# Kernel optimization log

Measured on AMD Instinct MI355X. Metric: run time of the kernel, lower is better.

The kernel has to match this reference:

```python
import jax, jax.numpy as jnp
import numpy as np

B, C, D = 16, 128, 256


def setup_inputs() -> dict:
    key = jax.random.key(0)
    ks = jax.random.split(key, 12)
    s = 0.05
    return {
        "h_t": jax.random.normal(ks[0], (B, C, D), jnp.float32),
        "A_a": jax.random.normal(ks[1], (C, C), jnp.float32) * s,
        "A_m": jax.random.normal(ks[2], (C, C), jnp.float32) * s,
        "W1": jax.random.normal(ks[3], (2 * D, D), jnp.float32) * s,
        "b1": jax.random.normal(ks[4], (D,), jnp.float32) * s,
        "W2": jax.random.normal(ks[5], (D, 1), jnp.float32) * s,
        "b2": jax.random.normal(ks[6], (1,), jnp.float32) * s,
        "Wa": jax.random.normal(ks[7], (D, D), jnp.float32) * s,
        "ba": jax.random.normal(ks[8], (D,), jnp.float32) * s,
        "Wm": jax.random.normal(ks[9], (D, D), jnp.float32) * s,
        "bm": jax.random.normal(ks[10], (D,), jnp.float32) * s,
        "beta1": jnp.float32(1.0),
        "beta2": jnp.float32(1.0),
        "beta3": jnp.float32(1.0),
    }


def reference(h_t, A_a, A_m, W1, b1, W2, b2, Wa, ba, Wm, bm, beta1, beta2, beta3):
    d = h_t.shape[-1]
    # Pairwise edge-MLP score S[b,u,v] = sigmoid(W2 @ relu(W1 @ [h_u; h_v] + b1) + b2).
    # Split W1 into the half acting on h_u and the half acting on h_v, so the
    # (B,C,C,2D) concat never materializes (same math as Linear on the concat).
    pre_u = jnp.einsum('bud,dk->buk', h_t, W1[:d])        # (B,C,D)
    pre_v = jnp.einsum('bvd,dk->bvk', h_t, W1[d:])        # (B,C,D)
    hidden = jax.nn.relu(pre_u[:, :, None, :] + pre_v[:, None, :, :] + b1)  # (B,C,C,D)
    S = jax.nn.sigmoid(jnp.einsum('buvk,ko->buvo', hidden, W2)[..., 0] + b2[0])  # (B,C,C)

    # Additive aggregation: a_t[b,v,:] = sum_u (S*A_a)[b,u,v] * h_t[b,u,:]
    a_t = jnp.einsum('buv,bud->bvd', S * A_a, h_t)

    # Hadamard aggregation: m_t[b,v,d] = sum_u A_m[u,v] * h[b,u,d] * h[b,v,d]
    #                              = (A_m^T @ h_t) * h_t  (avoids (B,C,C,D) tensor)
    m_t = jnp.einsum('uv,bud->bvd', A_m, h_t) * h_t

    z_t = (beta1 * h_t
           + beta2 * (jnp.einsum('bvd,de->bve', a_t, Wa) + ba)
           + beta3 * (jnp.einsum('bvd,de->bve', m_t, Wm) + bm))
    return z_t
```

## Files before the change

### kernel.cpp

```cpp
#include <hip/hip_runtime.h>

#define B_ 16
#define C_ 128
#define D_ 256

__global__ __launch_bounds__(256) void k1_pq(const float* __restrict__ h,
                                             const float* __restrict__ W1,
                                             const float* __restrict__ b1,
                                             float* __restrict__ P,
                                             float* __restrict__ Q) {
  const int tid = threadIdx.x;
  const int col = blockIdx.x * 64 + (tid & 63);
  const int rbase = (tid >> 6) * 8;
  const int row0 = blockIdx.y * 32;
  __shared__ float hs[32][D_];
#pragma unroll
  for (int r = 0; r < 32; ++r) hs[r][tid] = h[(row0 + r) * D_ + tid];
  __syncthreads();

  const int c = col & 255;
  const float* Wcol = W1 + c + ((col & 256) << 8);

  float acc[8];
#pragma unroll
  for (int i = 0; i < 8; ++i) acc[i] = 0.f;

#pragma unroll 2
  for (int d = 0; d < D_; d += 4) {
    const float w0 = Wcol[(d + 0) * D_];
    const float w1 = Wcol[(d + 1) * D_];
    const float w2 = Wcol[(d + 2) * D_];
    const float w3 = Wcol[(d + 3) * D_];
#pragma unroll
    for (int i = 0; i < 8; ++i) {
      const float4 hv = *(const float4*)&hs[rbase + i][d];
      acc[i] = fmaf(hv.x, w0, acc[i]);
      acc[i] = fmaf(hv.y, w1, acc[i]);
      acc[i] = fmaf(hv.z, w2, acc[i]);
      acc[i] = fmaf(hv.w, w3, acc[i]);
    }
  }

  if (col < 256) {
#pragma unroll
    for (int i = 0; i < 8; ++i) P[(row0 + rbase + i) * D_ + c] = acc[i];
  } else {
    const float bb = b1[c];
#pragma unroll
    for (int i = 0; i < 8; ++i) Q[(row0 + rbase + i) * D_ + c] = acc[i] + bb;
  }
}

__global__ __launch_bounds__(256) void k2_s(const float* __restrict__ P,
                                            const float* __restrict__ Q,
                                            const float* __restrict__ W2,
                                            const float* __restrict__ b2,
                                            const float* __restrict__ Aa,
                                            float* __restrict__ SA) {
  const int b = blockIdx.z;
  const int u0 = blockIdx.x * 32;
  const int v0 = blockIdx.y * 32;
  const int tid = threadIdx.x;
  const int tx = tid & 15;
  const int ty = tid >> 4;
  __shared__ float Pl[32][258];
  __shared__ float Ql[32][258];
  const float* Pb = P + (b * C_ + u0) * D_;
  const float* Qb = Q + (b * C_ + v0) * D_;
#pragma unroll
  for (int r = 0; r < 32; ++r) {
    Pl[r][tid] = Pb[r * D_ + tid];
    Ql[r][tid] = Qb[r * D_ + tid];
  }
  __syncthreads();

  const int uu0 = 2 * ty, uu1 = uu0 + 1;
  const int vv0 = 2 * tx, vv1 = vv0 + 1;
  const float2* __restrict__ pr0 = (const float2*)&Pl[uu0][0];
  const float2* __restrict__ pr1 = (const float2*)&Pl[uu1][0];
  const float2* __restrict__ qr0 = (const float2*)&Ql[vv0][0];
  const float2* __restrict__ qr1 = (const float2*)&Ql[vv1][0];
  const float2* __restrict__ w2v = (const float2*)W2;

  float a00 = 0.f, a01 = 0.f, a10 = 0.f, a11 = 0.f;
#pragma unroll 4
  for (int kk = 0; kk < D_ / 2; ++kk) {
    const float2 w = w2v[kk];
    const float2 p0 = pr0[kk];
    const float2 p1 = pr1[kk];
    const float2 q0 = qr0[kk];
    const float2 q1 = qr1[kk];
    a00 = fmaf(fmaxf(p0.x + q0.x, 0.f), w.x, a00);
    a00 = fmaf(fmaxf(p0.y + q0.y, 0.f), w.y, a00);
    a01 = fmaf(fmaxf(p0.x + q1.x, 0.f), w.x, a01);
    a01 = fmaf(fmaxf(p0.y + q1.y, 0.f), w.y, a01);
    a10 = fmaf(fmaxf(p1.x + q0.x, 0.f), w.x, a10);
    a10 = fmaf(fmaxf(p1.y + q0.y, 0.f), w.y, a10);
    a11 = fmaf(fmaxf(p1.x + q1.x, 0.f), w.x, a11);
    a11 = fmaf(fmaxf(p1.y + q1.y, 0.f), w.y, a11);
  }
  const float bb = b2[0];
  const float s00 = 1.f / (1.f + __expf(-(a00 + bb)));
  const float s01 = 1.f / (1.f + __expf(-(a01 + bb)));
  const float s10 = 1.f / (1.f + __expf(-(a10 + bb)));
  const float s11 = 1.f / (1.f + __expf(-(a11 + bb)));
  float* SAb = SA + b * C_ * C_;
  SAb[(v0 + vv0) * C_ + (u0 + uu0)] = s00 * Aa[(u0 + uu0) * C_ + (v0 + vv0)];
  SAb[(v0 + vv1) * C_ + (u0 + uu0)] = s01 * Aa[(u0 + uu0) * C_ + (v0 + vv1)];
  SAb[(v0 + vv0) * C_ + (u0 + uu1)] = s10 * Aa[(u0 + uu1) * C_ + (v0 + vv0)];
  SAb[(v0 + vv1) * C_ + (u0 + uu1)] = s11 * Aa[(u0 + uu1) * C_ + (v0 + vv1)];
}

__global__ __launch_bounds__(256) void k3_agg(const float* __restrict__ SA,
                                              const float* __restrict__ Am,
                                              const float* __restrict__ h,
                                              float* __restrict__ AT,
                                              float* __restrict__ MT) {
  const int b = blockIdx.y;
  const int v0 = blockIdx.x * 4;
  const int tid = threadIdx.x;
  __shared__ float SAl[4][128];
  __shared__ float AmT[4][128];
  for (int i = tid; i < 4 * 128; i += 256) {
    const int r = i >> 7, u = i & 127;
    SAl[r][u] = SA[b * C_ * C_ + (v0 + r) * C_ + u];
    AmT[r][u] = Am[u * C_ + (v0 + r)];
  }
  __syncthreads();
  const float* hb = h + b * C_ * D_;
  float accA[4], accM[4];
#pragma unroll
  for (int r = 0; r < 4; ++r) { accA[r] = 0.f; accM[r] = 0.f; }
#pragma unroll 4
  for (int u = 0; u < C_; ++u) {
    const float hv = hb[u * D_ + tid];
#pragma unroll
    for (int r = 0; r < 4; ++r) {
      accA[r] = fmaf(SAl[r][u], hv, accA[r]);
      accM[r] = fmaf(AmT[r][u], hv, accM[r]);
    }
  }
#pragma unroll
  for (int r = 0; r < 4; ++r) {
    const float hvv = hb[(v0 + r) * D_ + tid];
    AT[(b * C_ + v0 + r) * D_ + tid] = accA[r];
    MT[(b * C_ + v0 + r) * D_ + tid] = accM[r] * hvv;
  }
}

__global__ __launch_bounds__(256) void k4_out(const float* __restrict__ h,
                                              const float* __restrict__ AT,
                                              const float* __restrict__ MT,
                                              const float* __restrict__ Wa,
                                              const float* __restrict__ ba,
                                              const float* __restrict__ Wm,
                                              const float* __restrict__ bm,
                                              const float* __restrict__ be1,
                                              const float* __restrict__ be2,
                                              const float* __restrict__ be3,
                                              float* __restrict__ z) {
  const int tid = threadIdx.x;
  const int col = blockIdx.x * 64 + (tid & 63);
  const int rbase = (tid >> 6) * 4;
  const int row0 = blockIdx.y * 16;
  __shared__ float As[16][D_];
  __shared__ float Ms[16][D_];
#pragma unroll
  for (int r = 0; r < 16; ++r) {
    As[r][tid] = AT[(row0 + r) * D_ + tid];
    Ms[r][tid] = MT[(row0 + r) * D_ + tid];
  }
  __syncthreads();

  const float* WaC = Wa + col;
  const float* WmC = Wm + col;
  float accA[4], accM[4];
#pragma unroll
  for (int i = 0; i < 4; ++i) { accA[i] = 0.f; accM[i] = 0.f; }

#pragma unroll 2
  for (int d = 0; d < D_; d += 4) {
    const float wa0 = WaC[(d + 0) * D_];
    const float wa1 = WaC[(d + 1) * D_];
    const float wa2 = WaC[(d + 2) * D_];
    const float wa3 = WaC[(d + 3) * D_];
    const float wm0 = WmC[(d + 0) * D_];
    const float wm1 = WmC[(d + 1) * D_];
    const float wm2 = WmC[(d + 2) * D_];
    const float wm3 = WmC[(d + 3) * D_];
#pragma unroll
    for (int i = 0; i < 4; ++i) {
      const float4 av = *(const float4*)&As[rbase + i][d];
      const float4 mv = *(const float4*)&Ms[rbase + i][d];
      accA[i] = fmaf(av.x, wa0, accA[i]);
      accA[i] = fmaf(av.y, wa1, accA[i]);
      accA[i] = fmaf(av.z, wa2, accA[i]);
      accA[i] = fmaf(av.w, wa3, accA[i]);
      accM[i] = fmaf(mv.x, wm0, accM[i]);
      accM[i] = fmaf(mv.y, wm1, accM[i]);
      accM[i] = fmaf(mv.z, wm2, accM[i]);
      accM[i] = fmaf(mv.w, wm3, accM[i]);
    }
  }

  const float b1v = be1[0], b2v = be2[0], b3v = be3[0];
  const float bav = ba[col], bmv = bm[col];
#pragma unroll
  for (int i = 0; i < 4; ++i) {
    const int row = row0 + rbase + i;
    const float hv = h[row * D_ + col];
    z[row * D_ + col] = b1v * hv + b2v * (accA[i] + bav) + b3v * (accM[i] + bmv);
  }
}

extern "C" void kernel_launch(void* const* d_in, const int* in_sizes, int n_in,
                              void* d_out, int out_size, void* d_ws, size_t ws_size,
                              hipStream_t stream) {
  const float* h   = (const float*)d_in[0];
  const float* Aa  = (const float*)d_in[1];
  const float* Am  = (const float*)d_in[2];
  const float* W1  = (const float*)d_in[3];
  const float* b1  = (const float*)d_in[4];
  const float* W2  = (const float*)d_in[5];
  const float* b2  = (const float*)d_in[6];
  const float* Wa  = (const float*)d_in[7];
  const float* ba  = (const float*)d_in[8];
  const float* Wm  = (const float*)d_in[9];
  const float* bm  = (const float*)d_in[10];
  const float* be1 = (const float*)d_in[11];
  const float* be2 = (const float*)d_in[12];
  const float* be3 = (const float*)d_in[13];
  float* z = (float*)d_out;

  float* ws = (float*)d_ws;
  float* P  = ws;
  float* Q  = P + (B_ * C_ * D_);
  float* SA = Q + (B_ * C_ * D_);
  float* AT = SA + (B_ * C_ * C_);
  float* MT = AT + (B_ * C_ * D_);

  k1_pq <<<dim3(8, 64),    256, 0, stream>>>(h, W1, b1, P, Q);
  k2_s  <<<dim3(4, 4, 16), 256, 0, stream>>>(P, Q, W2, b2, Aa, SA);
  k3_agg<<<dim3(32, 16),   256, 0, stream>>>(SA, Am, h, AT, MT);
  k4_out<<<dim3(4, 128),   256, 0, stream>>>(h, AT, MT, Wa, ba, Wm, bm, be1, be2, be3, z);
}
```

Baseline: 142.8 us.

## Store P/Q in bf16 and shrink per-block tiles across all kernels

P and Q intermediates are now written as bf16 and unpacked in the edge-score kernel, halving their memory traffic. Every kernel is retiled to use smaller blocks and more of them (k1 8 rows, k2 16x16 with one output per thread, k3 2 rows, k4 8 rows x 128 columns). The aim is to raise occupancy and parallelism on a machine with many CUs. The costs are lower precision in the pre-activation sums and less register reuse per thread.

```diff
diff --git a/kernel.cpp b/kernel.cpp
--- a/kernel.cpp
+++ b/kernel.cpp
@@ -1,114 +1,98 @@
 #include <hip/hip_runtime.h>
+#include <hip/hip_bf16.h>
 
 #define B_ 16
 #define C_ 128
 #define D_ 256
 
+typedef unsigned int uint32;
+
+__device__ __forceinline__ float2 bf2x(uint32 x) {
+  return make_float2(__uint_as_float(x << 16), __uint_as_float(x & 0xffff0000u));
+}
+
 __global__ __launch_bounds__(256) void k1_pq(const float* __restrict__ h,
                                              const float* __restrict__ W1,
                                              const float* __restrict__ b1,
-                                             float* __restrict__ P,
-                                             float* __restrict__ Q) {
-  const int tid = threadIdx.x;
-  const int col = blockIdx.x * 64 + (tid & 63);
-  const int rbase = (tid >> 6) * 8;
-  const int row0 = blockIdx.y * 32;
-  __shared__ float hs[32][D_];
-#pragma unroll
-  for (int r = 0; r < 32; ++r) hs[r][tid] = h[(row0 + r) * D_ + tid];
-  __syncthreads();
-
-  const int c = col & 255;
-  const float* Wcol = W1 + c + ((col & 256) << 8);
-
-  float acc[8];
-#pragma unroll
-  for (int i = 0; i < 8; ++i) acc[i] = 0.f;
-
-#pragma unroll 2
+                                             __hip_bfloat16* __restrict__ P,
+                                             __hip_bfloat16* __restrict__ Q) {
+  const int tid = threadIdx.x;
+  const int vcol = blockIdx.x * 128 + (tid & 127);
+  const int rb = (tid >> 7) * 4;
+  const int row0 = blockIdx.y * 8;
+  __shared__ float hs[8][D_];
+#pragma unroll
+  for (int r = 0; r < 8; ++r) hs[r][tid] = h[(row0 + r) * D_ + tid];
+  __syncthreads();
+
+  const int c = vcol & 255;
+  const float* Wcol = W1 + c + ((vcol & 256) << 8);
+
+  float acc[4] = {0.f, 0.f, 0.f, 0.f};
+#pragma unroll 4
   for (int d = 0; d < D_; d += 4) {
     const float w0 = Wcol[(d + 0) * D_];
     const float w1 = Wcol[(d + 1) * D_];
     const float w2 = Wcol[(d + 2) * D_];
     const float w3 = Wcol[(d + 3) * D_];
 #pragma unroll
-    for (int i = 0; i < 8; ++i) {
-      const float4 hv = *(const float4*)&hs[rbase + i][d];
-      acc[i] = fmaf(hv.x, w0, acc[i]);
-      acc[i] = fmaf(hv.y, w1, acc[i]);
-      acc[i] = fmaf(hv.z, w2, acc[i]);
-      acc[i] = fmaf(hv.w, w3, acc[i]);
+    for (int i = 0; i < 4; ++i) {
+      const float4 hv = *(const float4*)&hs[rb + i][d];
+      acc[i] = fmaf(hv.x, w0, fmaf(hv.y, w1, fmaf(hv.z, w2, fmaf(hv.w, w3, acc[i]))));
     }
   }
 
-  if (col < 256) {
-#pragma unroll
-    for (int i = 0; i < 8; ++i) P[(row0 + rbase + i) * D_ + c] = acc[i];
+  if (vcol < 256) {
+#pragma unroll
+    for (int i = 0; i < 4; ++i)
+      P[(row0 + rb + i) * D_ + c] = __float2bfloat16(acc[i]);
   } else {
     const float bb = b1[c];
 #pragma unroll
-    for (int i = 0; i < 8; ++i) Q[(row0 + rbase + i) * D_ + c] = acc[i] + bb;
-  }
-}
-
-__global__ __launch_bounds__(256) void k2_s(const float* __restrict__ P,
-                                            const float* __restrict__ Q,
+    for (int i = 0; i < 4; ++i)
+      Q[(row0 + rb + i) * D_ + c] = __float2bfloat16(acc[i] + bb);
+  }
+}
+
+__global__ __launch_bounds__(256) void k2_s(const __hip_bfloat16* __restrict__ P,
+                                            const __hip_bfloat16* __restrict__ Q,
                                             const float* __restrict__ W2,
                                             const float* __restrict__ b2,
                                             const float* __restrict__ Aa,
                                             float* __restrict__ SA) {
   const int b = blockIdx.z;
-  const int u0 = blockIdx.x * 32;
-  const int v0 = blockIdx.y * 32;
-  const int tid = threadIdx.x;
-  const int tx = tid & 15;
-  const int ty = tid >> 4;
-  __shared__ float Pl[32][258];
-  __shared__ float Ql[32][258];
-  const float* Pb = P + (b * C_ + u0) * D_;
-  const float* Qb = Q + (b * C_ + v0) * D_;
-#pragma unroll
-  for (int r = 0; r < 32; ++r) {
-    Pl[r][tid] = Pb[r * D_ + tid];
-    Ql[r][tid] = Qb[r * D_ + tid];
-  }
-  __syncthreads();
-
-  const int uu0 = 2 * ty, uu1 = uu0 + 1;
-  const int vv0 = 2 * tx, vv1 = vv0 + 1;
-  const float2* __restrict__ pr0 = (const float2*)&Pl[uu0][0];
-  const float2* __restrict__ pr1 = (const float2*)&Pl[uu1][0];
-  const float2* __restrict__ qr0 = (const float2*)&Ql[vv0][0];
-  const float2* __restrict__ qr1 = (const float2*)&Ql[vv1][0];
+  const int u0 = blockIdx.x * 16;
+  const int v0 = blockIdx.y * 16;
+  const int tid = threadIdx.x;
+  __shared__ uint32 Pl[16][129];
+  __shared__ uint32 Ql[16][129];
+  const uint32* Pg = (const uint32*)(P + (b * C_ + u0) * D_);
+  const uint32* Qg = (const uint32*)(Q + (b * C_ + v0) * D_);
+#pragma unroll
+  for (int i = 0; i < 8; ++i) {
+    const int idx = i * 256 + tid;
+    const int r = idx >> 7, kk = idx & 127;
+    Pl[r][kk] = Pg[r * 128 + kk];
+    Ql[r][kk] = Qg[r * 128 + kk];
+  }
+  __syncthreads();
+
+  const int ul = tid & 15;
+  const int vl = tid >> 4;
   const float2* __restrict__ w2v = (const float2*)W2;
 
-  float a00 = 0.f, a01 = 0.f, a10 = 0.f, a11 = 0.f;
-#pragma unroll 4
-  for (int kk = 0; kk < D_ / 2; ++kk) {
+  float a = 0.f;
+#pragma unroll 8
+  for (int kk = 0; kk < 128; ++kk) {
+    const float2 p = bf2x(Pl[ul][kk]);
+    const float2 q = bf2x(Ql[vl][kk]);
     const float2 w = w2v[kk];
-    const float2 p0 = pr0[kk];
-    const float2 p1 = pr1[kk];
-    const float2 q0 = qr0[kk];
-    const float2 q1 = qr1[kk];
-    a00 = fmaf(fmaxf(p0.x + q0.x, 0.f), w.x, a00);
-    a00 = fmaf(fmaxf(p0.y + q0.y, 0.f), w.y, a00);
-    a01 = fmaf(fmaxf(p0.x + q1.x, 0.f), w.x, a01);
-    a01 = fmaf(fmaxf(p0.y + q1.y, 0.f), w.y, a01);
-    a10 = fmaf(fmaxf(p1.x + q0.x, 0.f), w.x, a10);
-    a10 = fmaf(fmaxf(p1.y + q0.y, 0.f), w.y, a10);
-    a11 = fmaf(fmaxf(p1.x + q1.x, 0.f), w.x, a11);
-    a11 = fmaf(fmaxf(p1.y + q1.y, 0.f), w.y, a11);
-  }
-  const float bb = b2[0];
-  const float s00 = 1.f / (1.f + __expf(-(a00 + bb)));
-  const float s01 = 1.f / (1.f + __expf(-(a01 + bb)));
-  const float s10 = 1.f / (1.f + __expf(-(a10 + bb)));
-  const float s11 = 1.f / (1.f + __expf(-(a11 + bb)));
-  float* SAb = SA + b * C_ * C_;
-  SAb[(v0 + vv0) * C_ + (u0 + uu0)] = s00 * Aa[(u0 + uu0) * C_ + (v0 + vv0)];
-  SAb[(v0 + vv1) * C_ + (u0 + uu0)] = s01 * Aa[(u0 + uu0) * C_ + (v0 + vv1)];
-  SAb[(v0 + vv0) * C_ + (u0 + uu1)] = s10 * Aa[(u0 + uu1) * C_ + (v0 + vv0)];
-  SAb[(v0 + vv1) * C_ + (u0 + uu1)] = s11 * Aa[(u0 + uu1) * C_ + (v0 + vv1)];
+    a = fmaf(fmaxf(p.x + q.x, 0.f), w.x, a);
+    a = fmaf(fmaxf(p.y + q.y, 0.f), w.y, a);
+  }
+  const float s = 1.f / (1.f + __expf(-(a + b2[0])));
+  const int u = u0 + ul, v = v0 + vl;
+  SA[b * C_ * C_ + v * C_ + u] = s * Aa[u * C_ + v];
 }
 
 __global__ __launch_bounds__(256) void k3_agg(const float* __restrict__ SA,
@@ -117,35 +101,32 @@
                                               float* __restrict__ AT,
                                               float* __restrict__ MT) {
   const int b = blockIdx.y;
-  const int v0 = blockIdx.x * 4;
-  const int tid = threadIdx.x;
-  __shared__ float SAl[4][128];
-  __shared__ float AmT[4][128];
-  for (int i = tid; i < 4 * 128; i += 256) {
-    const int r = i >> 7, u = i & 127;
-    SAl[r][u] = SA[b * C_ * C_ + (v0 + r) * C_ + u];
-    AmT[r][u] = Am[u * C_ + (v0 + r)];
+  const int v0 = blockIdx.x * 2;
+  const int tid = threadIdx.x;
+  __shared__ float SAl[2][128];
+  __shared__ float AmT[2][128];
+  {
+    const int r = tid >> 7, uu = tid & 127;
+    SAl[r][uu] = SA[b * C_ * C_ + (v0 + r) * C_ + uu];
+    AmT[r][uu] = Am[uu * C_ + (v0 + r)];
   }
   __syncthreads();
   const float* hb = h + b * C_ * D_;
-  float accA[4], accM[4];
-#pragma unroll
-  for (int r = 0; r < 4; ++r) { accA[r] = 0.f; accM[r] = 0.f; }
-#pragma unroll 4
+  float a0 = 0.f, a1 = 0.f, m0 = 0.f, m1 = 0.f;
+#pragma unroll 8
   for (int u = 0; u < C_; ++u) {
     const float hv = hb[u * D_ + tid];
-#pragma unroll
-    for (int r = 0; r < 4; ++r) {
-      accA[r] = fmaf(SAl[r][u], hv, accA[r]);
-      accM[r] = fmaf(AmT[r][u], hv, accM[r]);
-    }
-  }
-#pragma unroll
-  for (int r = 0; r < 4; ++r) {
-    const float hvv = hb[(v0 + r) * D_ + tid];
-    AT[(b * C_ + v0 + r) * D_ + tid] = accA[r];
-    MT[(b * C_ + v0 + r) * D_ + tid] = accM[r] * hvv;
-  }
+    a0 = fmaf(SAl[0][u], hv, a0);
+    a1 = fmaf(SAl[1][u], hv, a1);
+    m0 = fmaf(AmT[0][u], hv, m0);
+    m1 = fmaf(AmT[1][u], hv, m1);
+  }
+  const float h0 = hb[(v0 + 0) * D_ + tid];
+  const float h1 = hb[(v0 + 1) * D_ + tid];
+  AT[(b * C_ + v0 + 0) * D_ + tid] = a0;
+  AT[(b * C_ + v0 + 1) * D_ + tid] = a1;
+  MT[(b * C_ + v0 + 0) * D_ + tid] = m0 * h0;
+  MT[(b * C_ + v0 + 1) * D_ + tid] = m1 * h1;
 }
 
 __global__ __launch_bounds__(256) void k4_out(const float* __restrict__ h,
@@ -160,13 +141,13 @@
                                               const float* __restrict__ be3,
                                               float* __restrict__ z) {
   const int tid = threadIdx.x;
-  const int col = blockIdx.x * 64 + (tid & 63);
-  const int rbase = (tid >> 6) * 4;
-  const int row0 = blockIdx.y * 16;
-  __shared__ float As[16][D_];
-  __shared__ float Ms[16][D_];
-#pragma unroll
-  for (int r = 0; r < 16; ++r) {
+  const int col = blockIdx.x * 128 + (tid & 127);
+  const int rb = (tid >> 7) * 4;
+  const int row0 = blockIdx.y * 8;
+  __shared__ float As[8][D_];
+  __shared__ float Ms[8][D_];
+#pragma unroll
+  for (int r = 0; r < 8; ++r) {
     As[r][tid] = AT[(row0 + r) * D_ + tid];
     Ms[r][tid] = MT[(row0 + r) * D_ + tid];
   }
@@ -174,11 +155,9 @@
 
   const float* WaC = Wa + col;
   const float* WmC = Wm + col;
-  float accA[4], accM[4];
-#pragma unroll
-  for (int i = 0; i < 4; ++i) { accA[i] = 0.f; accM[i] = 0.f; }
-
-#pragma unroll 2
+  float accA[4] = {0.f, 0.f, 0.f, 0.f};
+  float accM[4] = {0.f, 0.f, 0.f, 0.f};
+#pragma unroll 4
   for (int d = 0; d < D_; d += 4) {
     const float wa0 = WaC[(d + 0) * D_];
     const float wa1 = WaC[(d + 1) * D_];
@@ -190,16 +169,10 @@
     const float wm3 = WmC[(d + 3) * D_];
 #pragma unroll
     for (int i = 0; i < 4; ++i) {
-      const float4 av = *(const float4*)&As[rbase + i][d];
-      const float4 mv = *(const float4*)&Ms[rbase + i][d];
-      accA[i] = fmaf(av.x, wa0, accA[i]);
-      accA[i] = fmaf(av.y, wa1, accA[i]);
-      accA[i] = fmaf(av.z, wa2, accA[i]);
-      accA[i] = fmaf(av.w, wa3, accA[i]);
-      accM[i] = fmaf(mv.x, wm0, accM[i]);
-      accM[i] = fmaf(mv.y, wm1, accM[i]);
-      accM[i] = fmaf(mv.z, wm2, accM[i]);
-      accM[i] = fmaf(mv.w, wm3, accM[i]);
+      const float4 av = *(const float4*)&As[rb + i][d];
+      const float4 mv = *(const float4*)&Ms[rb + i][d];
+      accA[i] = fmaf(av.x, wa0, fmaf(av.y, wa1, fmaf(av.z, wa2, fmaf(av.w, wa3, accA[i]))));
+      accM[i] = fmaf(mv.x, wm0, fmaf(mv.y, wm1, fmaf(mv.z, wm2, fmaf(mv.w, wm3, accM[i]))));
     }
   }
 
@@ -207,7 +180,7 @@
   const float bav = ba[col], bmv = bm[col];
 #pragma unroll
   for (int i = 0; i < 4; ++i) {
-    const int row = row0 + rbase + i;
+    const int row = row0 + rb + i;
     const float hv = h[row * D_ + col];
     z[row * D_ + col] = b1v * hv + b2v * (accA[i] + bav) + b3v * (accM[i] + bmv);
   }
@@ -232,15 +205,15 @@
   const float* be3 = (const float*)d_in[13];
   float* z = (float*)d_out;
 
-  float* ws = (float*)d_ws;
-  float* P  = ws;
-  float* Q  = P + (B_ * C_ * D_);
-  float* SA = Q + (B_ * C_ * D_);
+  char* wsb = (char*)d_ws;
+  __hip_bfloat16* P = (__hip_bfloat16*)wsb;
+  __hip_bfloat16* Q = P + (B_ * C_ * D_);
+  float* SA = (float*)(wsb + 2 * (size_t)(B_ * C_ * D_) * 2);
   float* AT = SA + (B_ * C_ * C_);
   float* MT = AT + (B_ * C_ * D_);
 
-  k1_pq <<<dim3(8, 64),    256, 0, stream>>>(h, W1, b1, P, Q);
-  k2_s  <<<dim3(4, 4, 16), 256, 0, stream>>>(P, Q, W2, b2, Aa, SA);
-  k3_agg<<<dim3(32, 16),   256, 0, stream>>>(SA, Am, h, AT, MT);
-  k4_out<<<dim3(4, 128),   256, 0, stream>>>(h, AT, MT, Wa, ba, Wm, bm, be1, be2, be3, z);
-}
+  k1_pq <<<dim3(4, 256),   256, 0, stream>>>(h, W1, b1, P, Q);
+  k2_s  <<<dim3(8, 8, 16), 256, 0, stream>>>(P, Q, W2, b2, Aa, SA);
+  k3_agg<<<dim3(64, 16),   256, 0, stream>>>(SA, Am, h, AT, MT);
+  k4_out<<<dim3(2, 256),   256, 0, stream>>>(h, AT, MT, Wa, ba, Wm, bm, be1, be2, be3, z);
+}
```

Result: slower. 154.8 us (+8.4%).
